# Kernel tuning notes

Measured on AMD Instinct MI355X. Metric: run time of the kernel, lower is better.

## Reference

```python
import jax, jax.numpy as jnp
import numpy as np

NUM_HEADS = 12
HEAD_DIM = 64
HIDDEN = NUM_HEADS * HEAD_DIM


def setup_inputs() -> dict:
    key = jax.random.key(0)
    ks = jax.random.split(key, 10)
    B, S, N_ROT = 8, 1374, 1369
    s = 0.02
    return {
        "hidden_states": jax.random.normal(ks[0], (B, S, HIDDEN), jnp.float32),
        "sin": jax.random.normal(ks[1], (N_ROT, HEAD_DIM), jnp.float32),
        "cos": jax.random.normal(ks[2], (N_ROT, HEAD_DIM), jnp.float32),
        "Wq": jax.random.normal(ks[3], (HIDDEN, HIDDEN), jnp.float32) * s,
        "bq": jax.random.normal(ks[4], (HIDDEN,), jnp.float32) * s,
        "Wk": jax.random.normal(ks[5], (HIDDEN, HIDDEN), jnp.float32) * s,
        "Wv": jax.random.normal(ks[6], (HIDDEN, HIDDEN), jnp.float32) * s,
        "bv": jax.random.normal(ks[7], (HIDDEN,), jnp.float32) * s,
        "Wp": jax.random.normal(ks[8], (HIDDEN, HIDDEN), jnp.float32) * s,
        "bp": jax.random.normal(ks[9], (HIDDEN,), jnp.float32) * s,
    }


def _rotate_half(x):
    x1, x2 = jnp.split(x, 2, axis=-1)
    return jnp.concatenate([-x2, x1], axis=-1)


def _rope_apply(x, sin, cos):
    return x * cos + _rotate_half(x) * sin


def reference(hidden_states, sin, cos, Wq, bq, Wk, Wv, bv, Wp, bp):
    B, S, _ = hidden_states.shape
    scaling = HEAD_DIM ** -0.5

    def to_heads(x):  # [B,S,HIDDEN] -> [B,H,S,D]
        return x.reshape(B, S, NUM_HEADS, HEAD_DIM).transpose(0, 2, 1, 3)

    q = to_heads(hidden_states @ Wq.T + bq)
    k = to_heads(hidden_states @ Wk.T)  # no key bias (mask_k_bias)
    v = to_heads(hidden_states @ Wv.T + bv)

    # RoPE only on patch tokens (prefix = cls + register tokens untouched)
    prefix = S - sin.shape[-2]
    q = jnp.concatenate([q[:, :, :prefix], _rope_apply(q[:, :, prefix:], sin, cos)], axis=2)
    k = jnp.concatenate([k[:, :, :prefix], _rope_apply(k[:, :, prefix:], sin, cos)], axis=2)

    # eager attention: softmax in float32, no mask, no dropout (eval)
    scores = jnp.einsum("bhqd,bhkd->bhqk", q, k) * scaling
    probs = jax.nn.softmax(scores.astype(jnp.float32), axis=-1).astype(q.dtype)
    ctx = jnp.einsum("bhqk,bhkd->bqhd", probs, v).reshape(B, S, HIDDEN)
    return ctx @ Wp.T + bp
```

## Files before the change

### kernel.cpp

```cpp
#include <hip/hip_runtime.h>
#include <stdint.h>

typedef unsigned short u16;
typedef unsigned int u32;
typedef u16 u16x8 __attribute__((ext_vector_type(8)));
typedef __bf16 bf16x8 __attribute__((ext_vector_type(8)));
typedef float f32x4 __attribute__((ext_vector_type(4)));

#define S_LEN 1374
#define S_PAD 1408
#define PRE_TOK 5
#define HID 768
#define NH 12
#define MPAD 11008

__device__ __forceinline__ u16 f2bf(float f) {
    union { float f; u32 u; } v; v.f = f;
    u32 r = v.u + 0x7fffu + ((v.u >> 16) & 1u);
    return (u16)(r >> 16);
}
__device__ __forceinline__ bf16x8 as_bf(u16x8 v) { bf16x8 r; __builtin_memcpy(&r, &v, 16); return r; }
__device__ __forceinline__ bf16x8 lds_load8(const u16* p) {
    u16x8 t = *(const u16x8*)p;
    return as_bf(t);
}
__device__ __forceinline__ u32 cvtpk_bf16(float lo, float hi) {
    u32 r;
    asm("v_cvt_pk_bf16_f32 %0, %1, %2" : "=v"(r) : "v"(lo), "v"(hi));
    return r;
}
__device__ __forceinline__ float fexp2(float x) {
    float r;
    asm("v_exp_f32 %0, %1" : "=v"(r) : "v"(x));
    return r;
}
__device__ __forceinline__ void gload16(void* lds, const void* g) {
    unsigned int __attribute__((address_space(1)))* gp =
        (unsigned int __attribute__((address_space(1)))*)(unsigned long long)g;
    unsigned int __attribute__((address_space(3)))* lp =
        (unsigned int __attribute__((address_space(3)))*)(unsigned int)(unsigned long long)lds;
    __builtin_amdgcn_global_load_lds(gp, lp, 16, 0, 0);
}
__device__ __forceinline__ int xcd_swz(int orig, int nwg) {
    int qd = nwg >> 3, rd = nwg & 7;
    int xcd = orig & 7, rem = orig >> 3;
    return (xcd < rd ? xcd * (qd + 1) : rd * (qd + 1) + (xcd - rd) * qd) + rem;
}


__global__ __launch_bounds__(256) void pack_x(const float* __restrict__ X, u16* __restrict__ Xb) {
    size_t i = (size_t)blockIdx.x * 256 + threadIdx.x;
    size_t e = i * 8;
    const size_t TOT = (size_t)10992 * HID;
    u16x8 o = {0,0,0,0,0,0,0,0};
    if (e < TOT) {
        f32x4 a = *(const f32x4*)(X + e);
        f32x4 b = *(const f32x4*)(X + e + 4);
#pragma unroll
        for (int j = 0; j < 4; ++j) { o[j] = f2bf(a[j]); o[4 + j] = f2bf(b[j]); }
    }
    *(u16x8*)(Xb + e) = o;
}

__global__ __launch_bounds__(256) void pack_w(
    const float* __restrict__ Wq, const float* __restrict__ Wk, const float* __restrict__ Wv,
    const float* __restrict__ Wp, const float* __restrict__ bq, const float* __restrict__ bv,
    u16* __restrict__ wqkv, u16* __restrict__ wpb, float* __restrict__ bqkv)
{
    int g = blockIdx.x * 256 + threadIdx.x;
    const int QKV8 = 2304 * HID / 8;
    const int P8 = HID * HID / 8;
    if (g < QKV8) {
        int e = g * 8;
        int row = e / HID, col = e - row * HID;
        const float* src = (row < 768) ? (Wq + (size_t)row * HID + col)
                         : (row < 1536) ? (Wk + (size_t)(row - 768) * HID + col)
                                        : (Wv + (size_t)(row - 1536) * HID + col);
        u16x8 o;
#pragma unroll
        for (int j = 0; j < 8; ++j) o[j] = f2bf(src[j]);
        *(u16x8*)(wqkv + e) = o;
    } else if (g < QKV8 + P8) {
        int e = (g - QKV8) * 8;
        u16x8 o;
#pragma unroll
        for (int j = 0; j < 8; ++j) o[j] = f2bf(Wp[e + j]);
        *(u16x8*)(wpb + e) = o;
    }
    if (g < 288) {
        int e = g * 8;
#pragma unroll
        for (int j = 0; j < 8; ++j) {
            int c = e + j;
            bqkv[c] = (c < 768) ? bq[c] : (c < 1536 ? 0.f : bv[c - 1536]);
        }
    }
}


template <int EPI>
__global__ __launch_bounds__(256) void gemm_nt(
    const u16* __restrict__ A, const u16* __restrict__ B, const float* __restrict__ bias,
    float* __restrict__ Yf, u16* __restrict__ Qh, u16* __restrict__ Kh,
    u16* __restrict__ Yv, const float* __restrict__ SN, const float* __restrict__ CS,
    int N, int K, int nx, int nwg)
{
    __shared__ u16 As[128 * 64];
    __shared__ u16 Bs[128 * 64];
    int tid = threadIdx.x;
    int w = tid >> 6, l = tid & 63;
    int fr = l & 15, fg = l >> 4;
    int wg = xcd_swz(blockIdx.x, nwg);
    int col0 = (wg % nx) * 128;
    int row0 = (wg / nx) * 128;
    int wr = (w >> 1) * 64, wc = (w & 1) * 64;

    f32x4 zero4 = {0.f, 0.f, 0.f, 0.f};
    f32x4 acc[4][4];
#pragma unroll
    for (int m = 0; m < 4; ++m)
#pragma unroll
        for (int n = 0; n < 4; ++n) acc[m][n] = zero4;

    int srow[4], soff[4];
#pragma unroll
    for (int i = 0; i < 4; ++i) {
        int sbyte = (i * 4 + w) * 1024 + l * 16;
        int r = sbyte >> 7;
        int ir = (sbyte & 127) ^ ((r & 7) << 4);
        srow[i] = r; soff[i] = ir >> 1;
    }

    for (int kt = 0; kt < K; kt += 64) {
#pragma unroll
        for (int i = 0; i < 4; ++i) {
            int sb = (i * 4 + w) * 1024;
            gload16((char*)As + sb, A + (size_t)(row0 + srow[i]) * K + kt + soff[i]);
            gload16((char*)Bs + sb, B + (size_t)(col0 + srow[i]) * K + kt + soff[i]);
        }
        __syncthreads();
#pragma unroll
        for (int c = 0; c < 2; ++c) {
            bf16x8 af[4], bfr[4];
#pragma unroll
            for (int m = 0; m < 4; ++m) {
                int r = wr + m * 16 + fr;
                int byte_ = (c * 64 + fg * 16) ^ ((r & 7) << 4);
                af[m] = lds_load8(As + r * 64 + (byte_ >> 1));
            }
#pragma unroll
            for (int n = 0; n < 4; ++n) {
                int r = wc + n * 16 + fr;
                int byte_ = (c * 64 + fg * 16) ^ ((r & 7) << 4);
                bfr[n] = lds_load8(Bs + r * 64 + (byte_ >> 1));
            }
#pragma unroll
            for (int m = 0; m < 4; ++m)
#pragma unroll
                for (int n = 0; n < 4; ++n)
                    acc[m][n] = __builtin_amdgcn_mfma_f32_16x16x32_bf16(af[m], bfr[n], acc[m][n], 0, 0, 0);
        }
        __syncthreads();
    }

    if (EPI == 1) {
#pragma unroll
        for (int m = 0; m < 4; ++m)
#pragma unroll
            for (int n = 0; n < 4; ++n) {
                int gn = col0 + wc + n * 16 + fr;
                float bvv = bias[gn];
#pragma unroll
                for (int j = 0; j < 4; ++j) {
                    int gm = row0 + wr + m * 16 + fg * 4 + j;
                    if (gm < 10992) Yf[(size_t)gm * N + gn] = acc[m][n][j] + bvv;
                }
            }
    } else {
        int sect = col0 >= 1536 ? 2 : (col0 >= 768 ? 1 : 0);
        if (sect == 2) {
#pragma unroll
            for (int m = 0; m < 4; ++m)
#pragma unroll
                for (int n = 0; n < 4; ++n) {
                    int gn = col0 + wc + n * 16 + fr;
                    float bvv = bias[gn];
#pragma unroll
                    for (int j = 0; j < 4; ++j) {
                        int gm = row0 + wr + m * 16 + fg * 4 + j;
                        if (gm < 10992)
                            Yv[(size_t)gm * HID + (gn - 1536)] = f2bf(acc[m][n][j] + bvv);
                    }
                }
        } else {
            u16* H = sect ? Kh : Qh;
            const float QS = sect ? 1.f : 0.125f * 1.44269504088896f;
            int hh = ((col0 + wc) >> 6) - sect * NH;
            float bv4[4];
#pragma unroll
            for (int n = 0; n < 4; ++n) bv4[n] = bias[col0 + wc + n * 16 + fr];
#pragma unroll
            for (int m = 0; m < 4; ++m)
#pragma unroll
                for (int j = 0; j < 4; ++j) {
                    int gm = row0 + wr + m * 16 + fg * 4 + j;
                    if (gm < 10992) {
                        int b = gm / 1374, s = gm - b * 1374;
                        size_t ob = ((size_t)(b * NH + hh) * S_PAD + s) * 64;
#pragma unroll
                        for (int n2 = 0; n2 < 2; ++n2) {
                            int d = n2 * 16 + fr;
                            float v1 = acc[m][n2][j] + bv4[n2];
                            float v2 = acc[m][n2 + 2][j] + bv4[n2 + 2];
                            float a1 = v1, a2 = v2;
                            if (s >= PRE_TOK) {
                                size_t rr = (size_t)(s - PRE_TOK) * 64;
                                float c1 = CS[rr + d], s1 = SN[rr + d];
                                float c2 = CS[rr + d + 32], s2 = SN[rr + d + 32];
                                a1 = v1 * c1 - v2 * s1;
                                a2 = v2 * c2 + v1 * s2;
                            }
                            H[ob + d]      = f2bf(a1 * QS);
                            H[ob + d + 32] = f2bf(a2 * QS);
                        }
                    }
                }
        }
    }
}


__global__ __launch_bounds__(256) void v_pack(const u16* __restrict__ Yv, u16* __restrict__ Vt) {
    int st = blockIdx.x, bh = blockIdx.y;
    int b = bh / NH, h = bh - b * NH;
    int tid = threadIdx.x;
    int sl = tid >> 2, dg = (tid & 3) * 8;
    int s = st * 64 + sl;
    __shared__ u16 vtile[64 * 64];

    u16x8 a = {0,0,0,0,0,0,0,0}, a2 = {0,0,0,0,0,0,0,0};
    if (s < S_LEN) {
        size_t base = ((size_t)b * S_LEN + s) * HID + h * 64;
        a  = *(const u16x8*)(Yv + base + dg);
        a2 = *(const u16x8*)(Yv + base + 32 + dg);
    }
#pragma unroll
    for (int j = 0; j < 8; ++j) {
        vtile[(dg + j) * 64 + sl] = a[j];
        vtile[(32 + dg + j) * 64 + sl] = a2[j];
    }
    __syncthreads();
    int d = tid >> 2, so = (tid & 3) * 8;
    u16x8 ov0 = *(const u16x8*)(vtile + d * 64 + so);
    u16x8 ov1 = *(const u16x8*)(vtile + d * 64 + so + 32);
    size_t vrow = ((size_t)bh * 64 + d) * S_PAD + st * 64;
    *(u16x8*)(Vt + vrow + so) = ov0;
    *(u16x8*)(Vt + vrow + so + 32) = ov1;
}


#define FLASH_BODY(Kc, Vc, KsN, VsN, ktn, DO_STAGE, DO_MASK)                          \
    {                                                                                 \
        asm volatile("s_waitcnt vmcnt(0) lgkmcnt(0)" ::: "memory");                   \
        __syncthreads();                                                              \
        if (DO_STAGE) {                                                               \
            int k0n = (ktn) * 32;                                                     \
            gload16((char*)(KsN) + sb, Kb + (size_t)k0n * 64 + kfix);                 \
            gload16((char*)(VsN) + sb, Vb + (size_t)k0n + vfix);                      \
        }                                                                             \
        f32x4 sf[2][2];                                                               \
        __builtin_amdgcn_s_setprio(1);                                                \
        _Pragma("unroll")                                                             \
        for (int n = 0; n < 2; ++n) {                                                 \
            f32x4 q0a = zero4, q1a = zero4;                                           \
            _Pragma("unroll")                                                         \
            for (int c = 0; c < 2; ++c) {                                             \
                int byte_ = (c * 64 + fg * 16) ^ ((fr & 7) << 4);                     \
                bf16x8 kf = lds_load8((Kc) + (n * 16 + fr) * 64 + (byte_ >> 1));      \
                q0a = __builtin_amdgcn_mfma_f32_16x16x32_bf16(kf, qf[0][c], q0a, 0, 0, 0); \
                q1a = __builtin_amdgcn_mfma_f32_16x16x32_bf16(kf, qf[1][c], q1a, 0, 0, 0); \
            }                                                                         \
            sf[0][n] = q0a; sf[1][n] = q1a;                                           \
        }                                                                             \
        __builtin_amdgcn_s_setprio(0);                                                \
        if (DO_MASK) {                                                                \
            _Pragma("unroll")                                                         \
            for (int n = 0; n < 2; ++n)                                               \
                _Pragma("unroll")                                                     \
                for (int j = 0; j < 4; ++j)                                           \
                    if (1344 + 8 * fg + 4 * n + j >= S_LEN) {                         \
                        sf[0][n][j] = -1e30f; sf[1][n][j] = -1e30f;                   \
                    }                                                                 \
        }                                                                             \
        union PA { u32 w2[4]; bf16x8 v; } pa[2];                                      \
        _Pragma("unroll")                                                             \
        for (int qq = 0; qq < 2; ++qq) {                                              \
            _Pragma("unroll")                                                         \
            for (int n = 0; n < 2; ++n)                                               \
                _Pragma("unroll")                                                     \
                for (int j = 0; j < 4; ++j) sf[qq][n][j] = fexp2(sf[qq][n][j]);       \
            pa[qq].w2[0] = cvtpk_bf16(sf[qq][0][0], sf[qq][0][1]);                    \
            pa[qq].w2[1] = cvtpk_bf16(sf[qq][0][2], sf[qq][0][3]);                    \
            pa[qq].w2[2] = cvtpk_bf16(sf[qq][1][0], sf[qq][1][1]);                    \
            pa[qq].w2[3] = cvtpk_bf16(sf[qq][1][2], sf[qq][1][3]);                    \
        }                                                                             \
        __builtin_amdgcn_s_setprio(1);                                                \
        lsum0 = __builtin_amdgcn_mfma_f32_16x16x32_bf16(pa[0].v, ones, lsum0, 0, 0, 0); \
        lsum1 = __builtin_amdgcn_mfma_f32_16x16x32_bf16(pa[1].v, ones, lsum1, 0, 0, 0); \
        _Pragma("unroll")                                                             \
        for (int nd = 0; nd < 4; ++nd) {                                              \
            int byte_ = ((nd >> 1) * 64 + fg * 16) ^ ((fr & 7) << 4);                 \
            bf16x8 vf = lds_load8((Vc) + ((nd & 1) * 16 + fr) * 64 + (byte_ >> 1));   \
            octx[0][nd] = __builtin_amdgcn_mfma_f32_16x16x32_bf16(pa[0].v, vf, octx[0][nd], 0, 0, 0); \
            octx[1][nd] = __builtin_amdgcn_mfma_f32_16x16x32_bf16(pa[1].v, vf, octx[1][nd], 0, 0, 0); \
        }                                                                             \
        __builtin_amdgcn_s_setprio(0);                                                \
    }

__global__ __launch_bounds__(256, 4) void flash(
    const u16* __restrict__ Qh, const u16* __restrict__ Kh, const u16* __restrict__ Vt,
    u16* __restrict__ ctxO)
{
    int wg = (blockIdx.x & 7) * 132 + (blockIdx.x >> 3);
    int qt = wg % 11, bh = wg / 11;
    int b = bh / NH, h = bh - b * NH;
    int q0 = qt * 128;
    int tid = threadIdx.x, w = tid >> 6, l = tid & 63;
    int fr = l & 15, fg = l >> 4;

    __shared__ u16 Ks0[32 * 64], Ks1[32 * 64];
    __shared__ u16 Vs0[32 * 64], Vs1[32 * 64];

    const u16* Qb = Qh + (size_t)bh * S_PAD * 64;
    const u16* Kb = Kh + (size_t)bh * S_PAD * 64;
    const u16* Vb = Vt + (size_t)bh * 64 * S_PAD;

    bf16x8 qf[2][2];
#pragma unroll
    for (int qq = 0; qq < 2; ++qq) {
        int qrow = q0 + w * 32 + qq * 16 + fr;
#pragma unroll
        for (int c = 0; c < 2; ++c)
            qf[qq][c] = as_bf(*(const u16x8*)(Qb + (size_t)qrow * 64 + c * 32 + fg * 8));
    }

    u16x8 ones_u = {0x3F80, 0x3F80, 0x3F80, 0x3F80, 0x3F80, 0x3F80, 0x3F80, 0x3F80};
    bf16x8 ones = as_bf(ones_u);

    f32x4 zero4 = {0.f, 0.f, 0.f, 0.f};
    f32x4 octx[2][4];
#pragma unroll
    for (int qq = 0; qq < 2; ++qq)
#pragma unroll
        for (int nd = 0; nd < 4; ++nd) octx[qq][nd] = zero4;
    f32x4 lsum0 = zero4, lsum1 = zero4;

    int r = w * 8 + (l >> 3);
    int bb = (l & 7) * 16;
    int ir = bb ^ ((r & 7) << 4);
    int gk = ((r >> 2) & 3) * 8 + ((r >> 4) & 1) * 4 + (r & 3);
    int kfix = gk * 64 + (ir >> 1);
    int vfix = (r + (ir >> 6) * 32) * S_PAD + ((ir & 63) >> 1);
    int sb = w * 1024;

    gload16((char*)Ks0 + sb, Kb + kfix);
    gload16((char*)Vs0 + sb, Vb + vfix);

    for (int kt = 0; kt < 42; kt += 2) {
        FLASH_BODY(Ks0, Vs0, Ks1, Vs1, kt + 1, true, false);
        FLASH_BODY(Ks1, Vs1, Ks0, Vs0, kt + 2, true, false);
    }
    FLASH_BODY(Ks0, Vs0, Ks1, Vs1, 0, false, true);

#pragma unroll
    for (int qq = 0; qq < 2; ++qq)
#pragma unroll
        for (int j = 0; j < 4; ++j) {
            int q = q0 + w * 32 + qq * 16 + fg * 4 + j;
            if (q < S_LEN) {
                float lv = qq ? lsum1[j] : lsum0[j];
                float inv = 1.f / lv;
                size_t rowb = ((size_t)b * S_LEN + q) * HID + h * 64;
#pragma unroll
                for (int nd = 0; nd < 4; ++nd)
                    ctxO[rowb + nd * 16 + fr] = f2bf(octx[qq][nd][j] * inv);
            }
        }
}


extern "C" void kernel_launch(void* const* d_in, const int* in_sizes, int n_in,
                              void* d_out, int out_size, void* d_ws, size_t ws_size,
                              hipStream_t stream) {
    (void)in_sizes; (void)n_in; (void)out_size; (void)ws_size;
    const float* X  = (const float*)d_in[0];
    const float* SN = (const float*)d_in[1];
    const float* CS = (const float*)d_in[2];
    const float* Wq = (const float*)d_in[3];
    const float* bq = (const float*)d_in[4];
    const float* Wk = (const float*)d_in[5];
    const float* Wv = (const float*)d_in[6];
    const float* bv = (const float*)d_in[7];
    const float* Wp = (const float*)d_in[8];
    const float* bp = (const float*)d_in[9];
    float* OUT = (float*)d_out;
    char* ws = (char*)d_ws;

    u16*   xb   = (u16*)(ws);
    u16*   wqkv = (u16*)(ws + 16908288);
    u16*   wpb  = (u16*)(ws + 20447232);
    float* bqkv = (float*)(ws + 21626880);
    u16*   Yv   = (u16*)(ws + 21636096);
    u16*   Qh   = (u16*)(ws + 72360960);
    u16*   Kh   = (u16*)(ws + 89662464);
    u16*   Vt   = (u16*)(ws + 106963968);
    u16*   ctx  = xb;

    pack_x<<<4128, 256, 0, stream>>>(X, xb);
    pack_w<<<1152, 256, 0, stream>>>(Wq, Wk, Wv, Wp, bq, bv, wqkv, wpb, bqkv);
    gemm_nt<2><<<1548, 256, 0, stream>>>(xb, wqkv, bqkv, nullptr, Qh, Kh, Yv, SN, CS, 2304, 768, 18, 1548);
    v_pack<<<dim3(22, 96), 256, 0, stream>>>(Yv, Vt);
    flash<<<1056, 256, 0, stream>>>(Qh, Kh, Vt, ctx);
    gemm_nt<1><<<516, 256, 0, stream>>>(ctx, wpb, bp, OUT, nullptr, nullptr, nullptr, nullptr, nullptr, 768, 768, 6, 516);
}
```

Baseline: 183.4 us.

## Triple-buffer GEMM with 512-thread 256x128 tiles and prefetch pipeline

Replaces the single-buffered 128x128 GEMM with a 512-thread kernel that computes 256x128 tiles. A/B tiles rotate through three LDS buffers, with loads issued two k-steps ahead and synchronised by vmcnt waits and barriers. MFMA sections are wrapped in s_setprio so global-load latency overlaps with compute. The cost is much more LDS per block (144KB), which may limit occupancy below the requested two blocks per CU. Fewer blocks also means a coarser wave tail on the small projection GEMM.

```diff
diff --git a/kernel.cpp b/kernel.cpp
--- a/kernel.cpp
+++ b/kernel.cpp
@@ -98,21 +98,73 @@
 }
 
 
+#define STAGE8(NA, NB, kk)                                                             \
+    {                                                                                  \
+        _Pragma("unroll")                                                              \
+        for (int i = 0; i < 4; ++i) {                                                  \
+            int sby = (i * 512 + tid) * 16;                                            \
+            int r = sby >> 7;                                                          \
+            int ir = (sby & 127) ^ ((r & 7) << 4);                                     \
+            gload16((char*)(NA) + i * 8192 + w * 1024,                                 \
+                    A + (size_t)(row0 + r) * K + (kk) + (ir >> 1));                    \
+        }                                                                              \
+        _Pragma("unroll")                                                              \
+        for (int i = 0; i < 2; ++i) {                                                  \
+            int sby = (i * 512 + tid) * 16;                                            \
+            int r = sby >> 7;                                                          \
+            int ir = (sby & 127) ^ ((r & 7) << 4);                                     \
+            gload16((char*)(NB) + i * 8192 + w * 1024,                                 \
+                    B + (size_t)(col0 + r) * K + (kk) + (ir >> 1));                    \
+        }                                                                              \
+    }
+
+#define GBODY8(CA, CB, NA, NB, t)                                                      \
+    {                                                                                  \
+        if ((t) < nkt - 1) { asm volatile("s_waitcnt vmcnt(6)" ::: "memory"); }        \
+        else               { asm volatile("s_waitcnt vmcnt(0)" ::: "memory"); }        \
+        __builtin_amdgcn_s_barrier();                                                  \
+        asm volatile("" ::: "memory");                                                 \
+        if ((t) + 2 < nkt) STAGE8(NA, NB, ((t) + 2) * 64);                             \
+        _Pragma("unroll")                                                              \
+        for (int c = 0; c < 2; ++c) {                                                  \
+            bf16x8 af[4], bfr[4];                                                      \
+            _Pragma("unroll")                                                          \
+            for (int m = 0; m < 4; ++m) {                                              \
+                int r = wr + m * 16 + fr;                                              \
+                int byte_ = (c * 64 + fg * 16) ^ ((r & 7) << 4);                       \
+                af[m] = lds_load8((CA) + r * 64 + (byte_ >> 1));                       \
+            }                                                                          \
+            _Pragma("unroll")                                                          \
+            for (int n = 0; n < 4; ++n) {                                              \
+                int r = wc + n * 16 + fr;                                              \
+                int byte_ = (c * 64 + fg * 16) ^ ((r & 7) << 4);                       \
+                bfr[n] = lds_load8((CB) + r * 64 + (byte_ >> 1));                      \
+            }                                                                          \
+            __builtin_amdgcn_s_setprio(1);                                             \
+            _Pragma("unroll")                                                          \
+            for (int m = 0; m < 4; ++m)                                                \
+                _Pragma("unroll")                                                      \
+                for (int n = 0; n < 4; ++n)                                            \
+                    acc[m][n] = __builtin_amdgcn_mfma_f32_16x16x32_bf16(af[m], bfr[n], acc[m][n], 0, 0, 0); \
+            __builtin_amdgcn_s_setprio(0);                                             \
+        }                                                                              \
+    }
+
 template <int EPI>
-__global__ __launch_bounds__(256) void gemm_nt(
+__global__ __launch_bounds__(512, 2) void gemm8p(
     const u16* __restrict__ A, const u16* __restrict__ B, const float* __restrict__ bias,
     float* __restrict__ Yf, u16* __restrict__ Qh, u16* __restrict__ Kh,
     u16* __restrict__ Yv, const float* __restrict__ SN, const float* __restrict__ CS,
     int N, int K, int nx, int nwg)
 {
-    __shared__ u16 As[128 * 64];
-    __shared__ u16 Bs[128 * 64];
+    __shared__ u16 Ab0[256 * 64], Ab1[256 * 64], Ab2[256 * 64];
+    __shared__ u16 Bb0[128 * 64], Bb1[128 * 64], Bb2[128 * 64];
     int tid = threadIdx.x;
     int w = tid >> 6, l = tid & 63;
     int fr = l & 15, fg = l >> 4;
     int wg = xcd_swz(blockIdx.x, nwg);
     int col0 = (wg % nx) * 128;
-    int row0 = (wg / nx) * 128;
+    int row0 = (wg / nx) * 256;
     int wr = (w >> 1) * 64, wc = (w & 1) * 64;
 
     f32x4 zero4 = {0.f, 0.f, 0.f, 0.f};
@@ -122,45 +174,14 @@
 #pragma unroll
         for (int n = 0; n < 4; ++n) acc[m][n] = zero4;
 
-    int srow[4], soff[4];
-#pragma unroll
-    for (int i = 0; i < 4; ++i) {
-        int sbyte = (i * 4 + w) * 1024 + l * 16;
-        int r = sbyte >> 7;
-        int ir = (sbyte & 127) ^ ((r & 7) << 4);
-        srow[i] = r; soff[i] = ir >> 1;
-    }
-
-    for (int kt = 0; kt < K; kt += 64) {
-#pragma unroll
-        for (int i = 0; i < 4; ++i) {
-            int sb = (i * 4 + w) * 1024;
-            gload16((char*)As + sb, A + (size_t)(row0 + srow[i]) * K + kt + soff[i]);
-            gload16((char*)Bs + sb, B + (size_t)(col0 + srow[i]) * K + kt + soff[i]);
-        }
-        __syncthreads();
-#pragma unroll
-        for (int c = 0; c < 2; ++c) {
-            bf16x8 af[4], bfr[4];
-#pragma unroll
-            for (int m = 0; m < 4; ++m) {
-                int r = wr + m * 16 + fr;
-                int byte_ = (c * 64 + fg * 16) ^ ((r & 7) << 4);
-                af[m] = lds_load8(As + r * 64 + (byte_ >> 1));
-            }
-#pragma unroll
-            for (int n = 0; n < 4; ++n) {
-                int r = wc + n * 16 + fr;
-                int byte_ = (c * 64 + fg * 16) ^ ((r & 7) << 4);
-                bfr[n] = lds_load8(Bs + r * 64 + (byte_ >> 1));
-            }
-#pragma unroll
-            for (int m = 0; m < 4; ++m)
-#pragma unroll
-                for (int n = 0; n < 4; ++n)
-                    acc[m][n] = __builtin_amdgcn_mfma_f32_16x16x32_bf16(af[m], bfr[n], acc[m][n], 0, 0, 0);
-        }
-        __syncthreads();
+    const int nkt = K >> 6;
+    STAGE8(Ab0, Bb0, 0);
+    STAGE8(Ab1, Bb1, 64);
+
+    for (int tt = 0; tt < nkt; tt += 3) {
+        GBODY8(Ab0, Bb0, Ab2, Bb2, tt);
+        GBODY8(Ab1, Bb1, Ab0, Bb0, tt + 1);
+        GBODY8(Ab2, Bb2, Ab1, Bb1, tt + 2);
     }
 
     if (EPI == 1) {
@@ -418,8 +439,8 @@
 
     pack_x<<<4128, 256, 0, stream>>>(X, xb);
     pack_w<<<1152, 256, 0, stream>>>(Wq, Wk, Wv, Wp, bq, bv, wqkv, wpb, bqkv);
-    gemm_nt<2><<<1548, 256, 0, stream>>>(xb, wqkv, bqkv, nullptr, Qh, Kh, Yv, SN, CS, 2304, 768, 18, 1548);
+    gemm8p<2><<<774, 512, 0, stream>>>(xb, wqkv, bqkv, nullptr, Qh, Kh, Yv, SN, CS, 2304, 768, 18, 774);
     v_pack<<<dim3(22, 96), 256, 0, stream>>>(Yv, Vt);
     flash<<<1056, 256, 0, stream>>>(Qh, Kh, Vt, ctx);
-    gemm_nt<1><<<516, 256, 0, stream>>>(ctx, wpb, bp, OUT, nullptr, nullptr, nullptr, nullptr, nullptr, 768, 768, 6, 516);
-}
+    gemm8p<1><<<258, 512, 0, stream>>>(ctx, wpb, bp, OUT, nullptr, nullptr, nullptr, nullptr, nullptr, 768, 768, 6, 258);
+}
```

After: 197.3 us. +7.6%, slower.
